# Kernel optimization log

Measured on AMD Instinct MI355X. Metric: run time of the kernel, lower is better.

The kernel has to match this reference:

```python
import jax, jax.numpy as jnp
import numpy as np

N_NODES = 50000
N_EDGES = 800000
NEG_SLOPE = 0.2  # PyG GATConv default


def _gat_layer(x, src, dst, n, W, a_src, a_dst, b, concat):
    """One GATConv layer (PyG semantics, eval mode so attention dropout is off).

    x: [N, F_in], src/dst: [E'] (self loops included), W: [F_in, H*C],
    a_src/a_dst: [H, C], b: [H*C] if concat else [C].
    """
    H, C = a_src.shape
    h = (x @ W).reshape(n, H, C)                      # [N, H, C]
    al_s = jnp.sum(h * a_src, axis=-1)                # [N, H]
    al_d = jnp.sum(h * a_dst, axis=-1)                # [N, H]
    e = jax.nn.leaky_relu(al_s[src] + al_d[dst], NEG_SLOPE)  # [E', H]
    # numerically stable softmax over incoming edges of each dst node
    m = jax.lax.stop_gradient(jax.ops.segment_max(e, dst, num_segments=n))
    m = jnp.where(jnp.isfinite(m), m, 0.0)
    ex = jnp.exp(e - m[dst])                          # [E', H]
    denom = jax.ops.segment_sum(ex, dst, num_segments=n)     # [N, H]
    alpha = ex / denom[dst]                           # safe: self loops => denom > 0
    out = jax.ops.segment_sum(alpha[:, :, None] * h[src], dst, num_segments=n)  # [N,H,C]
    out = out.reshape(n, H * C) if concat else out.mean(axis=1)
    return out + b


def setup_inputs() -> dict:
    key = jax.random.key(0)
    ks = jax.random.split(key, 8)
    in_dim, hid, heads, out_dim = 256, 32, 8, 16
    x = jax.random.normal(ks[0], (N_NODES, in_dim), dtype=jnp.float32)
    edge_index = jax.random.randint(ks[1], (2, N_EDGES), 0, N_NODES, dtype=jnp.int64)
    s1 = 1.0 / np.sqrt(in_dim)
    s2 = 1.0 / np.sqrt(heads * hid)
    return {
        "x": x,
        "edge_index": edge_index,
        "W1": jax.random.normal(ks[2], (in_dim, heads * hid), dtype=jnp.float32) * s1,
        "a_src1": jax.random.normal(ks[3], (heads, hid), dtype=jnp.float32) * s2,
        "a_dst1": jax.random.normal(ks[4], (heads, hid), dtype=jnp.float32) * s2,
        "b1": jnp.zeros((heads * hid,), dtype=jnp.float32),
        "W2": jax.random.normal(ks[5], (heads * hid, out_dim), dtype=jnp.float32) * s2,
        "a_src2": jax.random.normal(ks[6], (1, out_dim), dtype=jnp.float32) * 0.25,
        "a_dst2": jax.random.normal(ks[7], (1, out_dim), dtype=jnp.float32) * 0.25,
        "b2": jnp.zeros((out_dim,), dtype=jnp.float32),
    }


def reference(x, edge_index, W1, a_src1, a_dst1, b1, W2, a_src2, a_dst2, b2):
    n = x.shape[0]
    loops = jnp.arange(n, dtype=edge_index.dtype)
    src = jnp.concatenate([edge_index[0], loops])  # add_self_loops (PyG default)
    dst = jnp.concatenate([edge_index[1], loops])
    h = jax.nn.relu(_gat_layer(x, src, dst, n, W1, a_src1, a_dst1, b1, concat=True))
    # F.dropout(p=0.5, training=False) -> identity in eval mode
    h = _gat_layer(h, src, dst, n, W2, a_src2, a_dst2, b2, concat=False)
    return jax.nn.log_softmax(h, axis=1)
```

## Files before the change

kernel.cpp:

```cpp
#include <hip/hip_runtime.h>
#include <hip/hip_bf16.h>


#define LRELU(x) ((x) > 0.f ? (x) : 0.2f * (x))

typedef __attribute__((ext_vector_type(8))) short short8;
typedef __attribute__((ext_vector_type(8))) unsigned short ushort8;
typedef __attribute__((ext_vector_type(4))) float f32x4;

__device__ inline unsigned short f2b(float f) {
    __hip_bfloat16 h = __float2bfloat16(f);
    return *reinterpret_cast<unsigned short*>(&h);
}
__device__ inline float b2f(unsigned short u) {
    __hip_bfloat16 h;
    *reinterpret_cast<unsigned short*>(&h) = u;
    return __bfloat162float(h);
}


__global__ void k_init_deg(int* deg, int n) {
    int i = blockIdx.x * blockDim.x + threadIdx.x;
    if (i < n) deg[i] = 1;
}

__global__ void k_hist(const int* __restrict__ dst, int* deg, int E) {
    int i = blockIdx.x * blockDim.x + threadIdx.x;
    if (i < E) atomicAdd(&deg[dst[i]], 1);
}

__global__ __launch_bounds__(256) void k_scanA(const int* __restrict__ deg,
                                               int* __restrict__ tmp,
                                               int* __restrict__ blocksum, int n) {
    __shared__ int sc[256];
    int b = blockIdx.x, t = threadIdx.x;
    int i = b * 256 + t;
    int v = (i < n) ? deg[i] : 0;
    sc[t] = v;
    __syncthreads();
    for (int off = 1; off < 256; off <<= 1) {
        int x = 0;
        if (t >= off) x = sc[t - off];
        __syncthreads();
        sc[t] += x;
        __syncthreads();
    }
    if (i < n) tmp[i] = sc[t] - v;
    if (t == 255) blocksum[b] = sc[255];
}

__global__ __launch_bounds__(256) void k_scanB(const int* __restrict__ blocksum,
                                               int* __restrict__ blockpre, int nb) {
    __shared__ int sc[256];
    int t = threadIdx.x;
    int v = (t < nb) ? blocksum[t] : 0;
    sc[t] = v;
    __syncthreads();
    for (int off = 1; off < 256; off <<= 1) {
        int x = 0;
        if (t >= off) x = sc[t - off];
        __syncthreads();
        sc[t] += x;
        __syncthreads();
    }
    if (t < nb) blockpre[t] = sc[t] - v;
}

__global__ __launch_bounds__(256) void k_scanC(const int* __restrict__ tmp,
                                               const int* __restrict__ blockpre,
                                               int* __restrict__ offs,
                                               int* __restrict__ cursor, int n, int P) {
    int b = blockIdx.x, t = threadIdx.x;
    int i = b * 256 + t;
    if (i < n) {
        int o = tmp[i] + blockpre[b];
        offs[i] = o;
        cursor[i] = o;
    }
    if (i == 0) offs[n] = P;
}

__global__ void k_scatter(const int* __restrict__ src, const int* __restrict__ dst,
                          int* cursor, int* __restrict__ csr, int E, int n) {
    int i = blockIdx.x * blockDim.x + threadIdx.x;
    int s, d;
    if (i < E) {
        s = src[i];
        d = dst[i];
    } else if (i < E + n) {
        s = i - E;
        d = s;
    } else {
        return;
    }
    int p = atomicAdd(&cursor[d], 1);
    csr[p] = s;
}


__global__ __launch_bounds__(256) void k_prepw(const float* __restrict__ W,
                                               unsigned short* __restrict__ Wt) {
    int k = blockIdx.x;
    int nn = threadIdx.x;
    Wt[nn * 256 + k] = f2b(W[k * 256 + nn]);
}


__global__ __launch_bounds__(256) void k_gemm1(const float* __restrict__ A,
                                               const unsigned short* __restrict__ Wt,
                                               unsigned short* __restrict__ h1b, int M) {
    __shared__ unsigned short As[128][40];
    __shared__ unsigned short Bs[128][40];
    int t = threadIdx.x;
    int r0 = blockIdx.x * 128, c0 = blockIdx.y * 128;
    int srow = t >> 1, shalf = t & 1;
    int lane = t & 63, w = t >> 6;
    int lane15 = lane & 15, quad = lane >> 4;
    int rbw = (w & 1) * 64, cbw = (w >> 1) * 64;

    f32x4 acc[4][4];
#pragma unroll
    for (int i = 0; i < 4; i++)
#pragma unroll
        for (int j = 0; j < 4; j++) acc[i][j] = (f32x4)0.f;

    for (int k0 = 0; k0 < 256; k0 += 32) {
        {
            int row = r0 + srow;
            ushort8 p0, p1;
            if (row < M) {
                const float4* sp = (const float4*)&A[(size_t)row * 256 + k0 + shalf * 16];
                float4 f0 = sp[0], f1 = sp[1], f2 = sp[2], f3 = sp[3];
                p0[0] = f2b(f0.x); p0[1] = f2b(f0.y); p0[2] = f2b(f0.z); p0[3] = f2b(f0.w);
                p0[4] = f2b(f1.x); p0[5] = f2b(f1.y); p0[6] = f2b(f1.z); p0[7] = f2b(f1.w);
                p1[0] = f2b(f2.x); p1[1] = f2b(f2.y); p1[2] = f2b(f2.z); p1[3] = f2b(f2.w);
                p1[4] = f2b(f3.x); p1[5] = f2b(f3.y); p1[6] = f2b(f3.z); p1[7] = f2b(f3.w);
            } else {
                p0 = (ushort8)0; p1 = (ushort8)0;
            }
            *(ushort8*)&As[srow][shalf * 16] = p0;
            *(ushort8*)&As[srow][shalf * 16 + 8] = p1;
            const ushort8* bp = (const ushort8*)&Wt[(size_t)(c0 + srow) * 256 + k0 + shalf * 16];
            *(ushort8*)&Bs[srow][shalf * 16] = bp[0];
            *(ushort8*)&Bs[srow][shalf * 16 + 8] = bp[1];
        }
        __syncthreads();
        short8 af[4], bf[4];
#pragma unroll
        for (int i = 0; i < 4; i++)
            af[i] = *(const short8*)&As[rbw + i * 16 + lane15][quad * 8];
#pragma unroll
        for (int j = 0; j < 4; j++)
            bf[j] = *(const short8*)&Bs[cbw + j * 16 + lane15][quad * 8];
#pragma unroll
        for (int i = 0; i < 4; i++)
#pragma unroll
            for (int j = 0; j < 4; j++)
                acc[i][j] = __builtin_amdgcn_mfma_f32_16x16x32_bf16(af[i], bf[j], acc[i][j], 0, 0, 0);
        __syncthreads();
    }
#pragma unroll
    for (int i = 0; i < 4; i++) {
        int rowb = r0 + rbw + i * 16 + quad * 4;
#pragma unroll
        for (int j = 0; j < 4; j++) {
            int col = c0 + cbw + j * 16 + lane15;
#pragma unroll
            for (int r = 0; r < 4; r++) {
                int row = rowb + r;
                if (row < M) h1b[(size_t)row * 256 + col] = f2b(acc[i][j][r]);
            }
        }
    }
}


__global__ __launch_bounds__(256) void k_al1(const unsigned short* __restrict__ h1b,
                                             const float* __restrict__ asrc,
                                             const float* __restrict__ adst,
                                             float* __restrict__ als,
                                             float* __restrict__ ald, int n) {
    int v = blockIdx.x * 4 + (threadIdx.x >> 6);
    if (v >= n) return;
    int lane = threadIdx.x & 63;
    const uint2* hp = (const uint2*)(h1b + (size_t)v * 256);
    uint2 pk = hp[lane];
    float f0 = __uint_as_float(pk.x << 16);
    float f1 = __uint_as_float(pk.x & 0xffff0000u);
    float f2 = __uint_as_float(pk.y << 16);
    float f3 = __uint_as_float(pk.y & 0xffff0000u);
    float4 a_s = ((const float4*)asrc)[lane];
    float4 a_d = ((const float4*)adst)[lane];
    float ps = f0 * a_s.x + f1 * a_s.y + f2 * a_s.z + f3 * a_s.w;
    float pd = f0 * a_d.x + f1 * a_d.y + f2 * a_d.z + f3 * a_d.w;
#pragma unroll
    for (int off = 1; off < 8; off <<= 1) {
        ps += __shfl_xor(ps, off, 64);
        pd += __shfl_xor(pd, off, 64);
    }
    if ((lane & 7) == 0) {
        int h = lane >> 3;
        als[v * 8 + h] = ps;
        ald[v * 8 + h] = pd;
    }
}


__global__ __launch_bounds__(128) void k_agg1(const int* __restrict__ csr,
                                              const int* __restrict__ offs,
                                              const float* __restrict__ als,
                                              const float* __restrict__ aldg,
                                              const unsigned short* __restrict__ h1b,
                                              const float* __restrict__ b1,
                                              unsigned short* __restrict__ x2b) {
    int v = blockIdx.x;
    int t = threadIdx.x;
    int start = offs[v];
    int deg = offs[v + 1] - start;
    __shared__ float aldv[8];
    __shared__ int su[32];
    __shared__ float ws[256];
    if (t < 8) aldv[t] = aldg[v * 8 + t];
    __syncthreads();
    int h = t >> 4;
    float a0 = 0.f, a1 = 0.f, wsum = 0.f;
    for (int base = 0; base < deg; base += 32) {
        int cnt = min(32, deg - base);
        if (base) __syncthreads();
        if (t < cnt) {
            int u = csr[start + base + t];
            su[t] = u;
            const float4* ap = (const float4*)(als + (size_t)u * 8);
            float4 x0 = ap[0], x1 = ap[1];
            float e0 = x0.x + aldv[0], e1 = x0.y + aldv[1];
            float e2 = x0.z + aldv[2], e3 = x0.w + aldv[3];
            float e4 = x1.x + aldv[4], e5 = x1.y + aldv[5];
            float e6 = x1.z + aldv[6], e7 = x1.w + aldv[7];
            ws[t * 8 + 0] = __expf(LRELU(e0));
            ws[t * 8 + 1] = __expf(LRELU(e1));
            ws[t * 8 + 2] = __expf(LRELU(e2));
            ws[t * 8 + 3] = __expf(LRELU(e3));
            ws[t * 8 + 4] = __expf(LRELU(e4));
            ws[t * 8 + 5] = __expf(LRELU(e5));
            ws[t * 8 + 6] = __expf(LRELU(e6));
            ws[t * 8 + 7] = __expf(LRELU(e7));
        }
        __syncthreads();
        for (int e = 0; e < cnt; e++) {
            float wv = ws[e * 8 + h];
            const unsigned int* hp = (const unsigned int*)(h1b + (size_t)su[e] * 256);
            unsigned int pk = hp[t];
            float f0 = __uint_as_float(pk << 16);
            float f1 = __uint_as_float(pk & 0xffff0000u);
            a0 += wv * f0;
            a1 += wv * f1;
            wsum += wv;
        }
    }
    const float2* b1v = (const float2*)b1;
    float2 bb = b1v[t];
    float inv = 1.0f / wsum;
    float o0 = a0 * inv + bb.x;
    float o1 = a1 * inv + bb.y;
    o0 = o0 > 0.f ? o0 : 0.f;
    o1 = o1 > 0.f ? o1 : 0.f;
    unsigned int opk = (unsigned int)f2b(o0) | ((unsigned int)f2b(o1) << 16);
    ((unsigned int*)(x2b + (size_t)v * 256))[t] = opk;
}


__global__ __launch_bounds__(256) void k_gemm2(const unsigned short* __restrict__ Xb,
                                               const float* __restrict__ W,
                                               const float* __restrict__ asrc,
                                               const float* __restrict__ adst,
                                               float* __restrict__ h2,
                                               float* __restrict__ als,
                                               float* __restrict__ ald, int n) {
    __shared__ float xs[16][260];
    __shared__ float ws[256 * 16];
    int t = threadIdx.x;
    int r0 = blockIdx.x * 16;
#pragma unroll
    for (int i = 0; i < 16; i++) ws[t + i * 256] = W[t + i * 256];
#pragma unroll
    for (int i = 0; i < 16; i++) {
        int row = r0 + i;
        xs[i][t] = (row < n) ? b2f(Xb[(size_t)row * 256 + t]) : 0.f;
    }
    __syncthreads();
    int nl = t >> 4, j = t & 15;
    float acc = 0.f;
    const float4* xv = (const float4*)&xs[nl][0];
#pragma unroll 8
    for (int k4 = 0; k4 < 64; k4++) {
        float4 a = xv[k4];
        int k = k4 * 4;
        acc += a.x * ws[k * 16 + j] + a.y * ws[(k + 1) * 16 + j] +
               a.z * ws[(k + 2) * 16 + j] + a.w * ws[(k + 3) * 16 + j];
    }
    int row = r0 + nl;
    float ps = acc * asrc[j], pd = acc * adst[j];
#pragma unroll
    for (int off = 8; off; off >>= 1) {
        ps += __shfl_down(ps, off, 16);
        pd += __shfl_down(pd, off, 16);
    }
    if (row < n) {
        h2[row * 16 + j] = acc;
        if (j == 0) {
            als[row] = ps;
            ald[row] = pd;
        }
    }
}


__global__ __launch_bounds__(256) void k_agg2(const int* __restrict__ csr,
                                              const int* __restrict__ offs,
                                              const float* __restrict__ als,
                                              const float* __restrict__ aldg,
                                              const float* __restrict__ h2,
                                              const float* __restrict__ b2,
                                              float* __restrict__ out, int n) {
    int v = blockIdx.x * 4 + (threadIdx.x >> 6);
    if (v >= n) return;
    int lane = threadIdx.x & 63;
    int start = offs[v];
    int deg = offs[v + 1] - start;
    float aldv = aldg[v];
    int c = lane & 15, q = lane >> 4;
    float acc = 0.f, wsum = 0.f;
    for (int e = q; e < deg; e += 4) {
        int u = csr[start + e];
        float x = als[u] + aldv;
        float wv = __expf(LRELU(x));
        acc += wv * h2[(size_t)u * 16 + c];
        wsum += wv;
    }
    acc += __shfl_xor(acc, 32, 64);
    acc += __shfl_xor(acc, 16, 64);
    wsum += __shfl_xor(wsum, 32, 64);
    wsum += __shfl_xor(wsum, 16, 64);
    float o = acc / wsum + b2[c];
    float mx = o;
#pragma unroll
    for (int off = 8; off; off >>= 1) mx = fmaxf(mx, __shfl_xor(mx, off, 16));
    float s = __expf(o - mx);
#pragma unroll
    for (int off = 8; off; off >>= 1) s += __shfl_xor(s, off, 16);
    float res = o - mx - __logf(s);
    if (q == 0) out[(size_t)v * 16 + c] = res;
}


extern "C" void kernel_launch(void* const* d_in, const int* in_sizes, int n_in,
                              void* d_out, int out_size, void* d_ws, size_t ws_size,
                              hipStream_t stream) {
    const float* x = (const float*)d_in[0];
    const int* ei = (const int*)d_in[1];
    const float* W1 = (const float*)d_in[2];
    const float* asrc1 = (const float*)d_in[3];
    const float* adst1 = (const float*)d_in[4];
    const float* b1 = (const float*)d_in[5];
    const float* W2 = (const float*)d_in[6];
    const float* asrc2 = (const float*)d_in[7];
    const float* adst2 = (const float*)d_in[8];
    const float* b2 = (const float*)d_in[9];
    float* out = (float*)d_out;

    int n = in_sizes[0] / 256;
    int E = in_sizes[1] / 2;
    int P = E + n;
    const int* src = ei;
    const int* dst = ei + E;
    int NB = (n + 255) / 256;

    char* p = (char*)d_ws;
    auto alloc = [&](size_t bytes) {
        void* r = (void*)p;
        p += (bytes + 255) & ~(size_t)255;
        return r;
    };
    unsigned short* h1b = (unsigned short*)alloc((size_t)n * 256 * 2);
    unsigned short* x2b = (unsigned short*)alloc((size_t)n * 256 * 2);
    unsigned short* W1t = (unsigned short*)alloc((size_t)256 * 256 * 2);
    float* als1 = (float*)alloc((size_t)n * 8 * 4);
    float* ald1 = (float*)alloc((size_t)n * 8 * 4);
    float* h2 = (float*)alloc((size_t)n * 16 * 4);
    float* als2 = (float*)alloc((size_t)n * 4);
    float* ald2 = (float*)alloc((size_t)n * 4);
    int* deg = (int*)alloc((size_t)n * 4);
    int* offs = (int*)alloc((size_t)(n + 1) * 4);
    int* cursor = (int*)alloc((size_t)n * 4);
    int* stmp = (int*)alloc((size_t)n * 4);
    int* blocksum = (int*)alloc((size_t)NB * 4);
    int* blockpre = (int*)alloc((size_t)NB * 4);
    int* csr = (int*)alloc((size_t)P * 4);

    k_init_deg<<<(n + 255) / 256, 256, 0, stream>>>(deg, n);
    k_hist<<<(E + 255) / 256, 256, 0, stream>>>(dst, deg, E);
    k_scanA<<<NB, 256, 0, stream>>>(deg, stmp, blocksum, n);
    k_scanB<<<1, 256, 0, stream>>>(blocksum, blockpre, NB);
    k_scanC<<<NB, 256, 0, stream>>>(stmp, blockpre, offs, cursor, n, P);
    k_scatter<<<(P + 255) / 256, 256, 0, stream>>>(src, dst, cursor, csr, E, n);

    k_prepw<<<256, 256, 0, stream>>>(W1, W1t);
    k_gemm1<<<dim3((n + 127) / 128, 2), 256, 0, stream>>>(x, W1t, h1b, n);
    k_al1<<<(n + 3) / 4, 256, 0, stream>>>(h1b, asrc1, adst1, als1, ald1, n);
    k_agg1<<<n, 128, 0, stream>>>(csr, offs, als1, ald1, h1b, b1, x2b);

    k_gemm2<<<(n + 15) / 16, 256, 0, stream>>>(x2b, W2, asrc2, adst2, h2, als2, ald2, n);
    k_agg2<<<(n + 3) / 4, 256, 0, stream>>>(csr, offs, als2, ald2, h2, b2, out, n);
}
```

Measured before the change: 368.3 us.

## Use MFMA for layer-2 GEMM, store h2 in bf16, transpose agg1 weights

Replaces the scalar shared-memory layer-2 GEMM with a bf16 MFMA 16x16x32 kernel using a pre-transposed bf16 W2. h2 is stored as bf16 to halve gather traffic in agg2. The agg1 attention weights move to a padded head-major shared layout with a 2x unrolled edge loop, and the degree init kernel becomes a memset with the self-loop +1 folded into the scan. bf16 h2 and bf16 W2 add rounding error.

After: 343.9 us. 6.6% less time.

```diff
diff --git a/kernel.cpp b/kernel.cpp
--- a/kernel.cpp
+++ b/kernel.cpp
@@ -19,15 +19,11 @@
 }
 
 
-__global__ void k_init_deg(int* deg, int n) {
-    int i = blockIdx.x * blockDim.x + threadIdx.x;
-    if (i < n) deg[i] = 1;
-}
-
 __global__ void k_hist(const int* __restrict__ dst, int* deg, int E) {
     int i = blockIdx.x * blockDim.x + threadIdx.x;
     if (i < E) atomicAdd(&deg[dst[i]], 1);
 }
+
 
 __global__ __launch_bounds__(256) void k_scanA(const int* __restrict__ deg,
                                                int* __restrict__ tmp,
@@ -35,7 +31,7 @@
     __shared__ int sc[256];
     int b = blockIdx.x, t = threadIdx.x;
     int i = b * 256 + t;
-    int v = (i < n) ? deg[i] : 0;
+    int v = (i < n) ? deg[i] + 1 : 0;
     sc[t] = v;
     __syncthreads();
     for (int off = 1; off < 256; off <<= 1) {
@@ -103,6 +99,13 @@
     int k = blockIdx.x;
     int nn = threadIdx.x;
     Wt[nn * 256 + k] = f2b(W[k * 256 + nn]);
+}
+
+__global__ __launch_bounds__(256) void k_prepw2(const float* __restrict__ W,
+                                                unsigned short* __restrict__ Wt) {
+    int nn = blockIdx.x;
+    int k = threadIdx.x;
+    Wt[nn * 256 + k] = f2b(W[k * 16 + nn]);
 }
 
 
@@ -219,7 +222,7 @@
     int deg = offs[v + 1] - start;
     __shared__ float aldv[8];
     __shared__ int su[32];
-    __shared__ float ws[256];
+    __shared__ float ws[8 * 33];
     if (t < 8) aldv[t] = aldg[v * 8 + t];
     __syncthreads();
     int h = t >> 4;
@@ -232,22 +235,19 @@
             su[t] = u;
             const float4* ap = (const float4*)(als + (size_t)u * 8);
             float4 x0 = ap[0], x1 = ap[1];
-            float e0 = x0.x + aldv[0], e1 = x0.y + aldv[1];
-            float e2 = x0.z + aldv[2], e3 = x0.w + aldv[3];
-            float e4 = x1.x + aldv[4], e5 = x1.y + aldv[5];
-            float e6 = x1.z + aldv[6], e7 = x1.w + aldv[7];
-            ws[t * 8 + 0] = __expf(LRELU(e0));
-            ws[t * 8 + 1] = __expf(LRELU(e1));
-            ws[t * 8 + 2] = __expf(LRELU(e2));
-            ws[t * 8 + 3] = __expf(LRELU(e3));
-            ws[t * 8 + 4] = __expf(LRELU(e4));
-            ws[t * 8 + 5] = __expf(LRELU(e5));
-            ws[t * 8 + 6] = __expf(LRELU(e6));
-            ws[t * 8 + 7] = __expf(LRELU(e7));
-        }
-        __syncthreads();
+            ws[0 * 33 + t] = __expf(LRELU(x0.x + aldv[0]));
+            ws[1 * 33 + t] = __expf(LRELU(x0.y + aldv[1]));
+            ws[2 * 33 + t] = __expf(LRELU(x0.z + aldv[2]));
+            ws[3 * 33 + t] = __expf(LRELU(x0.w + aldv[3]));
+            ws[4 * 33 + t] = __expf(LRELU(x1.x + aldv[4]));
+            ws[5 * 33 + t] = __expf(LRELU(x1.y + aldv[5]));
+            ws[6 * 33 + t] = __expf(LRELU(x1.z + aldv[6]));
+            ws[7 * 33 + t] = __expf(LRELU(x1.w + aldv[7]));
+        }
+        __syncthreads();
+#pragma unroll 2
         for (int e = 0; e < cnt; e++) {
-            float wv = ws[e * 8 + h];
+            float wv = ws[h * 33 + e];
             const unsigned int* hp = (const unsigned int*)(h1b + (size_t)su[e] * 256);
             unsigned int pk = hp[t];
             float f0 = __uint_as_float(pk << 16);
@@ -270,46 +270,40 @@
 
 
 __global__ __launch_bounds__(256) void k_gemm2(const unsigned short* __restrict__ Xb,
-                                               const float* __restrict__ W,
+                                               const unsigned short* __restrict__ W2t,
                                                const float* __restrict__ asrc,
                                                const float* __restrict__ adst,
-                                               float* __restrict__ h2,
+                                               unsigned short* __restrict__ h2b,
                                                float* __restrict__ als,
                                                float* __restrict__ ald, int n) {
-    __shared__ float xs[16][260];
-    __shared__ float ws[256 * 16];
     int t = threadIdx.x;
-    int r0 = blockIdx.x * 16;
-#pragma unroll
-    for (int i = 0; i < 16; i++) ws[t + i * 256] = W[t + i * 256];
-#pragma unroll
-    for (int i = 0; i < 16; i++) {
-        int row = r0 + i;
-        xs[i][t] = (row < n) ? b2f(Xb[(size_t)row * 256 + t]) : 0.f;
-    }
-    __syncthreads();
-    int nl = t >> 4, j = t & 15;
-    float acc = 0.f;
-    const float4* xv = (const float4*)&xs[nl][0];
-#pragma unroll 8
-    for (int k4 = 0; k4 < 64; k4++) {
-        float4 a = xv[k4];
-        int k = k4 * 4;
-        acc += a.x * ws[k * 16 + j] + a.y * ws[(k + 1) * 16 + j] +
-               a.z * ws[(k + 2) * 16 + j] + a.w * ws[(k + 3) * 16 + j];
-    }
-    int row = r0 + nl;
-    float ps = acc * asrc[j], pd = acc * adst[j];
-#pragma unroll
-    for (int off = 8; off; off >>= 1) {
-        ps += __shfl_down(ps, off, 16);
-        pd += __shfl_down(pd, off, 16);
-    }
-    if (row < n) {
-        h2[row * 16 + j] = acc;
-        if (j == 0) {
-            als[row] = ps;
-            ald[row] = pd;
+    int lane = t & 63, w = t >> 6;
+    int lane15 = lane & 15, quad = lane >> 4;
+    int row0 = blockIdx.x * 64 + w * 16;
+    f32x4 acc = (f32x4)0.f;
+#pragma unroll
+    for (int k0 = 0; k0 < 256; k0 += 32) {
+        short8 a = *(const short8*)&Xb[(size_t)(row0 + lane15) * 256 + k0 + quad * 8];
+        short8 b = *(const short8*)&W2t[lane15 * 256 + k0 + quad * 8];
+        acc = __builtin_amdgcn_mfma_f32_16x16x32_bf16(a, b, acc, 0, 0, 0);
+    }
+    float asv = asrc[lane15], adv = adst[lane15];
+#pragma unroll
+    for (int r = 0; r < 4; r++) {
+        int row = row0 + quad * 4 + r;
+        float hv = acc[r];
+        float ps = hv * asv, pd = hv * adv;
+#pragma unroll
+        for (int off = 1; off < 16; off <<= 1) {
+            ps += __shfl_xor(ps, off, 16);
+            pd += __shfl_xor(pd, off, 16);
+        }
+        if (row < n) {
+            h2b[(size_t)row * 16 + lane15] = f2b(hv);
+            if (lane15 == 0) {
+                als[row] = ps;
+                ald[row] = pd;
+            }
         }
     }
 }
@@ -319,7 +313,7 @@
                                               const int* __restrict__ offs,
                                               const float* __restrict__ als,
                                               const float* __restrict__ aldg,
-                                              const float* __restrict__ h2,
+                                              const unsigned short* __restrict__ h2b,
                                               const float* __restrict__ b2,
                                               float* __restrict__ out, int n) {
     int v = blockIdx.x * 4 + (threadIdx.x >> 6);
@@ -334,7 +328,7 @@
         int u = csr[start + e];
         float x = als[u] + aldv;
         float wv = __expf(LRELU(x));
-        acc += wv * h2[(size_t)u * 16 + c];
+        acc += wv * b2f(h2b[(size_t)u * 16 + c]);
         wsum += wv;
     }
     acc += __shfl_xor(acc, 32, 64);
@@ -384,9 +378,10 @@
     unsigned short* h1b = (unsigned short*)alloc((size_t)n * 256 * 2);
     unsigned short* x2b = (unsigned short*)alloc((size_t)n * 256 * 2);
     unsigned short* W1t = (unsigned short*)alloc((size_t)256 * 256 * 2);
+    unsigned short* W2t = (unsigned short*)alloc((size_t)16 * 256 * 2);
     float* als1 = (float*)alloc((size_t)n * 8 * 4);
     float* ald1 = (float*)alloc((size_t)n * 8 * 4);
-    float* h2 = (float*)alloc((size_t)n * 16 * 4);
+    unsigned short* h2b = (unsigned short*)alloc((size_t)n * 16 * 2);
     float* als2 = (float*)alloc((size_t)n * 4);
     float* ald2 = (float*)alloc((size_t)n * 4);
     int* deg = (int*)alloc((size_t)n * 4);
@@ -397,7 +392,7 @@
     int* blockpre = (int*)alloc((size_t)NB * 4);
     int* csr = (int*)alloc((size_t)P * 4);
 
-    k_init_deg<<<(n + 255) / 256, 256, 0, stream>>>(deg, n);
+    hipMemsetAsync(deg, 0, (size_t)n * 4, stream);
     k_hist<<<(E + 255) / 256, 256, 0, stream>>>(dst, deg, E);
     k_scanA<<<NB, 256, 0, stream>>>(deg, stmp, blocksum, n);
     k_scanB<<<1, 256, 0, stream>>>(blocksum, blockpre, NB);
@@ -405,10 +400,11 @@
     k_scatter<<<(P + 255) / 256, 256, 0, stream>>>(src, dst, cursor, csr, E, n);
 
     k_prepw<<<256, 256, 0, stream>>>(W1, W1t);
+    k_prepw2<<<16, 256, 0, stream>>>(W2, W2t);
     k_gemm1<<<dim3((n + 127) / 128, 2), 256, 0, stream>>>(x, W1t, h1b, n);
     k_al1<<<(n + 3) / 4, 256, 0, stream>>>(h1b, asrc1, adst1, als1, ald1, n);
     k_agg1<<<n, 128, 0, stream>>>(csr, offs, als1, ald1, h1b, b1, x2b);
 
-    k_gemm2<<<(n + 15) / 16, 256, 0, stream>>>(x2b, W2, asrc2, adst2, h2, als2, ald2, n);
-    k_agg2<<<(n + 3) / 4, 256, 0, stream>>>(csr, offs, als2, ald2, h2, b2, out, n);
-}
+    k_gemm2<<<(n + 63) / 64, 256, 0, stream>>>(x2b, W2t, asrc2, adst2, h2b, als2, ald2, n);
+    k_agg2<<<(n + 3) / 4, 256, 0, stream>>>(csr, offs, als2, ald2, h2b, b2, out, n);
+}
```
